# Performance work log

Hardware: AMD Instinct MI355X
Metric: run time of the kernel (lower is better)

The kernel has to match this reference:

```python
import jax, jax.numpy as jnp
import numpy as np

HEAD_DIM = 32
N_HEADS = 8
Q_DIM = 128
FF_DIM = 4 * Q_DIM
EPS = 1e-5


def layernorm(x, gamma, beta):
    mu = jnp.mean(x, axis=-1, keepdims=True)
    var = jnp.var(x, axis=-1, keepdims=True)
    return (x - mu) * jax.lax.rsqrt(var + EPS) * gamma + beta


def setup_inputs() -> dict:
    key = jax.random.key(0)
    ks = jax.random.split(key, 20)
    S, B = 1024, 16
    sc_in = 1.0 / np.sqrt(Q_DIM)
    sc_hd = 1.0 / np.sqrt(N_HEADS * HEAD_DIM)
    sc_ff = 1.0 / np.sqrt(FF_DIM)
    return {
        "sequence": jax.random.normal(ks[0], (S, B, Q_DIM), jnp.float32),
        # per-head Q/K/V projections, stacked over heads: [H, Q_dim, head_dim]
        "Wq": jax.random.uniform(ks[1], (N_HEADS, Q_DIM, HEAD_DIM), jnp.float32, -sc_in, sc_in),
        "bq": jax.random.uniform(ks[2], (N_HEADS, HEAD_DIM), jnp.float32, -sc_in, sc_in),
        "Wk": jax.random.uniform(ks[3], (N_HEADS, Q_DIM, HEAD_DIM), jnp.float32, -sc_in, sc_in),
        "bk": jax.random.uniform(ks[4], (N_HEADS, HEAD_DIM), jnp.float32, -sc_in, sc_in),
        "Wv": jax.random.uniform(ks[5], (N_HEADS, Q_DIM, HEAD_DIM), jnp.float32, -sc_in, sc_in),
        "bv": jax.random.uniform(ks[6], (N_HEADS, HEAD_DIM), jnp.float32, -sc_in, sc_in),
        # post_head_linear: [H*head_dim, Q_dim]
        "Wo": jax.random.uniform(ks[7], (N_HEADS * HEAD_DIM, Q_DIM), jnp.float32, -sc_hd, sc_hd),
        "bo": jax.random.uniform(ks[8], (Q_DIM,), jnp.float32, -sc_hd, sc_hd),
        # norm1 (note: original reuses norm1 for both layernorms)
        "gamma1": jnp.ones((Q_DIM,), jnp.float32),
        "beta1": jnp.zeros((Q_DIM,), jnp.float32),
        # FFN: Q_dim -> 4Q -> 4Q -> Q_dim
        "W1": jax.random.uniform(ks[9], (Q_DIM, FF_DIM), jnp.float32, -sc_in, sc_in),
        "b1": jax.random.uniform(ks[10], (FF_DIM,), jnp.float32, -sc_in, sc_in),
        "W2": jax.random.uniform(ks[11], (FF_DIM, FF_DIM), jnp.float32, -sc_ff, sc_ff),
        "b2": jax.random.uniform(ks[12], (FF_DIM,), jnp.float32, -sc_ff, sc_ff),
        "W3": jax.random.uniform(ks[13], (FF_DIM, Q_DIM), jnp.float32, -sc_ff, sc_ff),
        "b3": jax.random.uniform(ks[14], (Q_DIM,), jnp.float32, -sc_ff, sc_ff),
    }


def reference(sequence, Wq, bq, Wk, bk, Wv, bv, Wo, bo, gamma1, beta1, W1, b1, W2, b2, W3, b3):
    # sequence: [S, B, Q_dim] -> batch-first [B, S, Q_dim]
    x = jnp.transpose(sequence, (1, 0, 2))
    # batched per-head projections: [B, H, S, d]
    q = jnp.einsum('bsq,hqd->bhsd', x, Wq) + bq[None, :, None, :]
    k = jnp.einsum('bsq,hqd->bhsd', x, Wk) + bk[None, :, None, :]
    v = jnp.einsum('bsq,hqd->bhsd', x, Wv) + bv[None, :, None, :]
    scores = jnp.einsum('bhsd,bhtd->bhst', q, k) / np.sqrt(HEAD_DIM)
    attn = jax.nn.softmax(scores, axis=-1)
    o = jnp.einsum('bhst,bhtd->bhsd', attn, v)  # [B, H, S, d]
    B, H, S, d = o.shape
    o = jnp.transpose(o, (0, 2, 1, 3)).reshape(B, S, H * d)  # concat heads
    att_outs = o @ Wo + bo
    att_outs = layernorm(x + att_outs, gamma1, beta1)
    h = jax.nn.relu(att_outs @ W1 + b1)
    h = jax.nn.relu(h @ W2 + b2)
    h = h @ W3 + b3
    out = layernorm(att_outs + h, gamma1, beta1)  # original reuses norm1
    return jnp.transpose(out, (1, 0, 2))  # back to [S, B, Q_dim]
```

## Files before the change

kernel.cpp:

```cpp
#include <hip/hip_runtime.h>
#include <hip/hip_bf16.h>

#define S_LEN 1024
#define BATCH 16
#define QD 128
#define NH 8
#define HD 32
#define FF 512
#define NROWS (BATCH * S_LEN)
#define EPS 1e-5f

typedef __attribute__((ext_vector_type(4))) float f32x4;
typedef __attribute__((ext_vector_type(8))) short s16x8;
typedef __attribute__((ext_vector_type(4))) short s16x4;

__device__ __forceinline__ ushort f2bfu(float f) {
    union { float f; unsigned u; } v; v.f = f;
    unsigned r = (v.u + 0x7FFFu + ((v.u >> 16) & 1u)) >> 16;
    return (ushort)r;
}

__device__ __forceinline__ float exp2_fast(float x) {
#if __has_builtin(__builtin_amdgcn_exp2f)
    return __builtin_amdgcn_exp2f(x);
#else
    float r;
    asm("v_exp_f32 %0, %1" : "=v"(r) : "v"(x));
    return r;
#endif
}

__device__ __forceinline__ unsigned pk_bf16(float a, float b) {
    union { __hip_bfloat162 h; unsigned u; } c;
    c.h = __float22bfloat162_rn(make_float2(a, b));
    return c.u;
}

static __device__ __forceinline__ f32x4 mfma16(s16x4 a, s16x4 b, f32x4 c) {
#if __has_builtin(__builtin_amdgcn_mfma_f32_16x16x16bf16_1k)
    return __builtin_amdgcn_mfma_f32_16x16x16bf16_1k(a, b, c, 0, 0, 0);
#else
    asm volatile("v_mfma_f32_16x16x16_bf16 %0, %1, %2, %0" : "+v"(c) : "v"(a), "v"(b));
    return c;
#endif
}

static __device__ __forceinline__ f32x4 mfma32(s16x8 a, s16x8 b, f32x4 c) {
    return __builtin_amdgcn_mfma_f32_16x16x32_bf16(a, b, c, 0, 0, 0);
}

__device__ __forceinline__ void gl_lds16(const void* g, void* l) {
    __builtin_amdgcn_global_load_lds(
        (const __attribute__((address_space(1))) void*)g,
        (__attribute__((address_space(3))) void*)l, 16, 0, 0);
}

template <int K>
__device__ __forceinline__ void gemm_core(
    const ushort* __restrict__ act, const ushort* __restrict__ WTp,
    char* lds, int tok0, f32x4 acc[8]) {
    const int tid = threadIdx.x;
    const int w = tid >> 6, lane = tid & 63;
    const int qi = lane & 15, g = lane >> 4;
    const int r8 = tid >> 3;
    const int csw = (tid & 7) ^ (r8 & 7);
    const int wave_base = w * 1024;
    constexpr int NT = K / 64;

    auto STAGE = [&](int b, int ks) {
        char* buf = lds + b * 24576;
#pragma unroll
        for (int i = 0; i < 4; ++i)
            gl_lds16(WTp + (size_t)(i * 32 + r8) * K + ks + csw * 8,
                     buf + i * 4096 + wave_base);
#pragma unroll
        for (int j = 0; j < 2; ++j)
            gl_lds16(act + (size_t)(tok0 + j * 32 + r8) * K + ks + csw * 8,
                     buf + 16384 + j * 4096 + wave_base);
    };

    STAGE(0, 0);
    int cur = 0;
#pragma unroll 1
    for (int t = 0; t < NT; ++t) {
        if (t < NT - 1) {
            STAGE(cur ^ 1, (t + 1) * 64);
            asm volatile("s_waitcnt vmcnt(6)" ::: "memory");
        } else {
            asm volatile("s_waitcnt vmcnt(0)" ::: "memory");
        }
        __builtin_amdgcn_sched_barrier(0);
        __builtin_amdgcn_s_barrier();
        __builtin_amdgcn_sched_barrier(0);
        const char* A = lds + cur * 24576;
        const char* B = A + 16384;
        const int brow = w * 16 + qi;
        __builtin_amdgcn_s_setprio(1);
#pragma unroll
        for (int kk2 = 0; kk2 < 2; ++kk2) {
            s16x8 bfrag = *(const s16x8*)(B + brow * 128 +
                                          (((kk2 * 4 + g) ^ (brow & 7)) * 16));
#pragma unroll
            for (int f = 0; f < 8; ++f) {
                const int row = qi + 16 * f;
                s16x8 afrag = *(const s16x8*)(A + row * 128 +
                                              (((kk2 * 4 + g) ^ (row & 7)) * 16));
                acc[f] = mfma32(afrag, bfrag, acc[f]);
            }
        }
        __builtin_amdgcn_s_setprio(0);
        __builtin_amdgcn_sched_barrier(0);
        __builtin_amdgcn_s_barrier();
        __builtin_amdgcn_sched_barrier(0);
        cur ^= 1;
    }
}

__global__ __launch_bounds__(256) void prep_weights(
    const float* __restrict__ Wo, const float* __restrict__ W1,
    const float* __restrict__ W2, const float* __restrict__ W3,
    const float* __restrict__ Wq, const float* __restrict__ Wk,
    const float* __restrict__ Wv,
    ushort* __restrict__ WoT, ushort* __restrict__ W1T,
    ushort* __restrict__ W2T, ushort* __restrict__ W3T,
    ushort* __restrict__ WqkvT) {
    int idx = blockIdx.x * 256 + threadIdx.x;
    if (idx < 32768) {
        int n = idx >> 8, k = idx & 255;
        WoT[n * 256 + k] = f2bfu(Wo[k * 128 + n]);
    } else if (idx < 98304) {
        int i = idx - 32768; int n = i >> 7, k = i & 127;
        W1T[n * 128 + k] = f2bfu(W1[k * 512 + n]);
    } else if (idx < 360448) {
        int i = idx - 98304; int n = i >> 9, k = i & 511;
        W2T[n * 512 + k] = f2bfu(W2[k * 512 + n]);
    } else if (idx < 425984) {
        int i = idx - 360448; int n = i >> 9, k = i & 511;
        W3T[n * 512 + k] = f2bfu(W3[k * 128 + n]);
    } else {
        int i = idx - 425984;
        int n = i >> 7, k = i & 127;
        int p = n >> 8, h = (n >> 5) & 7, d = n & 31;
        const float* W = (p == 0) ? Wq : (p == 1) ? Wk : Wv;
        WqkvT[n * 128 + k] = f2bfu(W[(h * QD + k) * HD + d]);
    }
}

__global__ __launch_bounds__(256) void seq2bf(
    const float* __restrict__ seq, ushort* __restrict__ x_bf) {
    int t = blockIdx.x * 256 + threadIdx.x;
    int e4 = t * 4;
    int s = e4 >> 11, b = (e4 >> 7) & 15, c = e4 & 127;
    float4 v = *(const float4*)(seq + e4);
    ushort4 o = {f2bfu(v.x), f2bfu(v.y), f2bfu(v.z), f2bfu(v.w)};
    *(ushort4*)(x_bf + ((size_t)(b * 1024 + s)) * 128 + c) = o;
}

__global__ __launch_bounds__(256) void qkv_mfma(
    const ushort* __restrict__ x_bf, const ushort* __restrict__ WqkvT,
    const float* __restrict__ bq, const float* __restrict__ bk,
    const float* __restrict__ bv,
    ushort* __restrict__ q_bf, ushort* __restrict__ k_bf,
    ushort* __restrict__ vT) {
    __shared__ __align__(16) char lds[2 * 24576];
    const int lane = threadIdx.x & 63;
    const int w = threadIdx.x >> 6;
    const int qi = lane & 15, g = lane >> 4;
    const int tok0 = blockIdx.x * 64;
    const int tok = tok0 + w * 16 + qi;
    const int n0 = blockIdx.y * 128;

    f32x4 acc[8];
#pragma unroll
    for (int f = 0; f < 8; ++f) acc[f] = (f32x4){0.f, 0.f, 0.f, 0.f};
    gemm_core<128>(x_bf, WqkvT + (size_t)n0 * 128, lds, tok0, acc);

    const int b = tok >> 10, s = tok & 1023;
    const float SCALE = 0.25503491f;
    if (n0 < 256) {
#pragma unroll
        for (int f = 0; f < 8; ++f)
#pragma unroll
            for (int r = 0; r < 4; ++r) {
                int n = n0 + 16 * f + 4 * g + r;
                int h = (n >> 5) & 7, d = n & 31;
                q_bf[((size_t)(b * 8 + h) * 1024 + s) * 32 + d] =
                    f2bfu((acc[f][r] + bq[h * 32 + d]) * SCALE);
            }
    } else if (n0 < 512) {
#pragma unroll
        for (int f = 0; f < 8; ++f)
#pragma unroll
            for (int r = 0; r < 4; ++r) {
                int n = n0 + 16 * f + 4 * g + r;
                int h = (n >> 5) & 7, d = n & 31;
                k_bf[((size_t)(b * 8 + h) * 1024 + s) * 32 + d] =
                    f2bfu(acc[f][r] + bk[h * 32 + d]);
            }
    } else {
#pragma unroll
        for (int f = 0; f < 8; ++f)
#pragma unroll
            for (int r = 0; r < 4; ++r) {
                int n = n0 + 16 * f + 4 * g + r;
                int h = (n >> 5) & 7, d = n & 31;
                vT[((size_t)(b * 8 + h) * 32 + d) * 1024 + s] =
                    f2bfu(acc[f][r] + bv[h * 32 + d]);
            }
    }
}

__global__ __launch_bounds__(256) void attn_mfma(
    const ushort* __restrict__ qb, const ushort* __restrict__ kb,
    const ushort* __restrict__ vtb, ushort* __restrict__ o_bf) {
    __shared__ __align__(16) char lds[2][8192];
    const int tid = threadIdx.x;
    const int w = tid >> 6, lane = tid & 63;
    const int g = lane >> 4, qi = lane & 15;
    const int bid = blockIdx.x;
    const int swz = (bid & 7) * 256 + (bid >> 3);
    const int bh = swz >> 4;
    const int qtile = (swz & 15) * 4 + w;

    const ushort* Kb = kb + (size_t)bh * S_LEN * HD;
    const ushort* VTb = vtb + (size_t)bh * HD * S_LEN;
    const s16x8 qf = *(const s16x8*)(qb + ((size_t)bh * S_LEN + qtile * 16 + qi) * HD + g * 8);

    const int krow = tid >> 2;
    const int ksw = (tid & 3) ^ ((tid >> 3) & 3);
    const int vrow = tid >> 3;
    const int vsw = (tid & 7) ^ ((tid >> 4) & 7);
    const int wave_off = w * 1024;

#define STAGE(bufp, k0)                                                          \
    do {                                                                         \
        gl_lds16(Kb + (size_t)((k0) + krow) * HD + ksw * 8, (bufp) + wave_off);  \
        gl_lds16(VTb + (size_t)vrow * S_LEN + (k0) + vsw * 8,                    \
                 (bufp) + 4096 + wave_off);                                      \
    } while (0)

    f32x4 ot0 = {0.f, 0.f, 0.f, 0.f};
    f32x4 ot1 = {0.f, 0.f, 0.f, 0.f};
    float m_run = -1e30f, l_run = 0.f;
    const f32x4 zero = {0.f, 0.f, 0.f, 0.f};

    const int koff = (g ^ ((qi >> 1) & 3)) * 16;
    const int vs = (qi >> 1) & 7;

    STAGE(lds[0], 0);
    int cur = 0;
#pragma unroll 1
    for (int t = 0; t < 16; ++t) {
        if (t < 15) {
            STAGE(lds[cur ^ 1], (t + 1) * 64);
            asm volatile("s_waitcnt vmcnt(2)" ::: "memory");
        } else {
            asm volatile("s_waitcnt vmcnt(0)" ::: "memory");
        }
        __builtin_amdgcn_sched_barrier(0);
        __builtin_amdgcn_s_barrier();
        __builtin_amdgcn_sched_barrier(0);

        const char* kl = lds[cur];
        const char* vl = lds[cur] + 4096;
        s16x8 ka[4];
#pragma unroll
        for (int kt = 0; kt < 4; ++kt)
            ka[kt] = *(const s16x8*)(kl + (16 * kt + qi) * 64 + koff);
        s16x4 va[2][4];
#pragma unroll
        for (int h = 0; h < 2; ++h)
#pragma unroll
            for (int kt = 0; kt < 4; ++kt) {
                int c8 = 4 * kt + g;
                va[h][kt] = *(const s16x4*)(vl + (16 * h + qi) * 128 +
                                            (((c8 >> 1) ^ vs) * 16) + (c8 & 1) * 8);
            }

        f32x4 st[4];
        __builtin_amdgcn_s_setprio(1);
#pragma unroll
        for (int kt = 0; kt < 4; ++kt) st[kt] = mfma32(ka[kt], qf, zero);
        __builtin_amdgcn_s_setprio(0);

        float a0 = fmaxf(fmaxf(st[0][0], st[0][1]), fmaxf(st[0][2], st[0][3]));
        float a1 = fmaxf(fmaxf(st[1][0], st[1][1]), fmaxf(st[1][2], st[1][3]));
        float a2 = fmaxf(fmaxf(st[2][0], st[2][1]), fmaxf(st[2][2], st[2][3]));
        float a3 = fmaxf(fmaxf(st[3][0], st[3][1]), fmaxf(st[3][2], st[3][3]));
        float pmax = fmaxf(fmaxf(a0, a1), fmaxf(a2, a3));

        if (!__all(pmax <= m_run + 8.0f)) {
            float mt = pmax;
            mt = fmaxf(mt, __shfl_xor(mt, 16, 64));
            mt = fmaxf(mt, __shfl_xor(mt, 32, 64));
            float m_new = fmaxf(m_run, mt);
            float alpha = exp2_fast(m_run - m_new);
            l_run *= alpha;
#pragma unroll
            for (int r = 0; r < 4; ++r) { ot0[r] *= alpha; ot1[r] *= alpha; }
            m_run = m_new;
        }

        float p[4][4];
#pragma unroll
        for (int kt = 0; kt < 4; ++kt)
#pragma unroll
            for (int r = 0; r < 4; ++r) p[kt][r] = exp2_fast(st[kt][r] - m_run);
        float s0 = (p[0][0] + p[0][1]) + (p[0][2] + p[0][3]);
        float s1 = (p[1][0] + p[1][1]) + (p[1][2] + p[1][3]);
        float s2 = (p[2][0] + p[2][1]) + (p[2][2] + p[2][3]);
        float s3 = (p[3][0] + p[3][1]) + (p[3][2] + p[3][3]);
        l_run += (s0 + s1) + (s2 + s3);

        union { s16x4 v; uint2 u; } pb[4];
#pragma unroll
        for (int kt = 0; kt < 4; ++kt) {
            pb[kt].u.x = pk_bf16(p[kt][0], p[kt][1]);
            pb[kt].u.y = pk_bf16(p[kt][2], p[kt][3]);
        }
        __builtin_amdgcn_s_setprio(1);
#pragma unroll
        for (int kt = 0; kt < 4; ++kt) {
            ot0 = mfma16(va[0][kt], pb[kt].v, ot0);
            ot1 = mfma16(va[1][kt], pb[kt].v, ot1);
        }
        __builtin_amdgcn_s_setprio(0);

        __builtin_amdgcn_sched_barrier(0);
        __builtin_amdgcn_s_barrier();
        __builtin_amdgcn_sched_barrier(0);
        cur ^= 1;
    }
#undef STAGE

    l_run += __shfl_xor(l_run, 16, 64);
    l_run += __shfl_xor(l_run, 32, 64);
    const float inv_l = 1.0f / l_run;
    const int b = bh >> 3, head = bh & 7;
    const int qg = qtile * 16 + qi;
    ushort* orow = o_bf + ((size_t)(b * S_LEN + qg)) * (NH * HD) + head * HD;
    ushort4 ob0 = {f2bfu(ot0[0] * inv_l), f2bfu(ot0[1] * inv_l),
                   f2bfu(ot0[2] * inv_l), f2bfu(ot0[3] * inv_l)};
    ushort4 ob1 = {f2bfu(ot1[0] * inv_l), f2bfu(ot1[1] * inv_l),
                   f2bfu(ot1[2] * inv_l), f2bfu(ot1[3] * inv_l)};
    *(ushort4*)(orow + g * 4) = ob0;
    *(ushort4*)(orow + 16 + g * 4) = ob1;
}

__global__ __launch_bounds__(256) void wo_ln_mfma(
    const ushort* __restrict__ o_bf, const ushort* __restrict__ WoT,
    const float* __restrict__ bo, const float* __restrict__ seq,
    const float* __restrict__ gamma, const float* __restrict__ beta,
    float* __restrict__ att, ushort* __restrict__ att_bf) {
    __shared__ __align__(16) char lds[2 * 24576];
    const int lane = threadIdx.x & 63;
    const int w = threadIdx.x >> 6;
    const int qi = lane & 15, g = lane >> 4;
    const int tok0 = blockIdx.x * 64;
    const int tok = tok0 + w * 16 + qi;

    f32x4 acc[8];
#pragma unroll
    for (int f = 0; f < 8; ++f) acc[f] = (f32x4){0.f, 0.f, 0.f, 0.f};
    gemm_core<256>(o_bf, WoT, lds, tok0, acc);

    const int b = tok >> 10, s = tok & 1023;
    const float* xrow = seq + (size_t)(s * BATCH + b) * QD;
    float sum = 0.f, sumsq = 0.f;
#pragma unroll
    for (int f = 0; f < 8; ++f) {
        const int c = 16 * f + 4 * g;
        float4 bv = *(const float4*)(bo + c);
        float4 xv = *(const float4*)(xrow + c);
        acc[f][0] += bv.x + xv.x;
        acc[f][1] += bv.y + xv.y;
        acc[f][2] += bv.z + xv.z;
        acc[f][3] += bv.w + xv.w;
#pragma unroll
        for (int r = 0; r < 4; ++r) { sum += acc[f][r]; sumsq += acc[f][r] * acc[f][r]; }
    }
    sum += __shfl_xor(sum, 16, 64);
    sum += __shfl_xor(sum, 32, 64);
    sumsq += __shfl_xor(sumsq, 16, 64);
    sumsq += __shfl_xor(sumsq, 32, 64);
    const float mu = sum * (1.0f / QD);
    const float var = sumsq * (1.0f / QD) - mu * mu;
    const float rstd = rsqrtf(var + EPS);

#pragma unroll
    for (int f = 0; f < 8; ++f) {
        const int c = 16 * f + 4 * g;
        float4 gm = *(const float4*)(gamma + c);
        float4 bt = *(const float4*)(beta + c);
        float4 ov;
        ov.x = (acc[f][0] - mu) * rstd * gm.x + bt.x;
        ov.y = (acc[f][1] - mu) * rstd * gm.y + bt.y;
        ov.z = (acc[f][2] - mu) * rstd * gm.z + bt.z;
        ov.w = (acc[f][3] - mu) * rstd * gm.w + bt.w;
        *(float4*)(att + (size_t)tok * QD + c) = ov;
        ushort4 pv = {f2bfu(ov.x), f2bfu(ov.y), f2bfu(ov.z), f2bfu(ov.w)};
        *(ushort4*)(att_bf + (size_t)tok * QD + c) = pv;
    }
}

template <int K>
__global__ __launch_bounds__(256) void ffn_mfma(
    const ushort* __restrict__ act, const ushort* __restrict__ WT,
    const float* __restrict__ bias, ushort* __restrict__ out, int N) {
    __shared__ __align__(16) char lds[2 * 24576];
    const int lane = threadIdx.x & 63;
    const int w = threadIdx.x >> 6;
    const int qi = lane & 15, g = lane >> 4;
    const int tok0 = blockIdx.x * 64;
    const int tok = tok0 + w * 16 + qi;
    const int n0 = blockIdx.y * 128;

    f32x4 acc[8];
#pragma unroll
    for (int f = 0; f < 8; ++f) acc[f] = (f32x4){0.f, 0.f, 0.f, 0.f};
    gemm_core<K>(act, WT + (size_t)n0 * K, lds, tok0, acc);

#pragma unroll
    for (int f = 0; f < 8; ++f) {
        const int c = n0 + 16 * f + 4 * g;
        float4 bv = *(const float4*)(bias + c);
        ushort4 pv;
        pv.x = f2bfu(fmaxf(acc[f][0] + bv.x, 0.f));
        pv.y = f2bfu(fmaxf(acc[f][1] + bv.y, 0.f));
        pv.z = f2bfu(fmaxf(acc[f][2] + bv.z, 0.f));
        pv.w = f2bfu(fmaxf(acc[f][3] + bv.w, 0.f));
        *(ushort4*)(out + (size_t)tok * N + c) = pv;
    }
}

__global__ __launch_bounds__(256) void w3_ln_mfma(
    const ushort* __restrict__ h2, const ushort* __restrict__ W3T,
    const float* __restrict__ b3, const float* __restrict__ att,
    const float* __restrict__ gamma, const float* __restrict__ beta,
    float* __restrict__ out) {
    __shared__ __align__(16) char lds[2 * 24576];
    const int lane = threadIdx.x & 63;
    const int w = threadIdx.x >> 6;
    const int qi = lane & 15, g = lane >> 4;
    const int tok0 = blockIdx.x * 64;
    const int tok = tok0 + w * 16 + qi;

    f32x4 acc[8];
#pragma unroll
    for (int f = 0; f < 8; ++f) acc[f] = (f32x4){0.f, 0.f, 0.f, 0.f};
    gemm_core<512>(h2, W3T, lds, tok0, acc);

    float sum = 0.f, sumsq = 0.f;
#pragma unroll
    for (int f = 0; f < 8; ++f) {
        const int c = 16 * f + 4 * g;
        float4 bv = *(const float4*)(b3 + c);
        float4 xv = *(const float4*)(att + (size_t)tok * QD + c);
        acc[f][0] += bv.x + xv.x;
        acc[f][1] += bv.y + xv.y;
        acc[f][2] += bv.z + xv.z;
        acc[f][3] += bv.w + xv.w;
#pragma unroll
        for (int r = 0; r < 4; ++r) { sum += acc[f][r]; sumsq += acc[f][r] * acc[f][r]; }
    }
    sum += __shfl_xor(sum, 16, 64);
    sum += __shfl_xor(sum, 32, 64);
    sumsq += __shfl_xor(sumsq, 16, 64);
    sumsq += __shfl_xor(sumsq, 32, 64);
    const float mu = sum * (1.0f / QD);
    const float var = sumsq * (1.0f / QD) - mu * mu;
    const float rstd = rsqrtf(var + EPS);

    const int b = tok >> 10, s = tok & 1023;
    float* orow = out + (size_t)(s * BATCH + b) * QD;
#pragma unroll
    for (int f = 0; f < 8; ++f) {
        const int c = 16 * f + 4 * g;
        float4 gm = *(const float4*)(gamma + c);
        float4 bt = *(const float4*)(beta + c);
        float4 ov;
        ov.x = (acc[f][0] - mu) * rstd * gm.x + bt.x;
        ov.y = (acc[f][1] - mu) * rstd * gm.y + bt.y;
        ov.z = (acc[f][2] - mu) * rstd * gm.z + bt.z;
        ov.w = (acc[f][3] - mu) * rstd * gm.w + bt.w;
        *(float4*)(orow + c) = ov;
    }
}

extern "C" void kernel_launch(void* const* d_in, const int* in_sizes, int n_in,
                              void* d_out, int out_size, void* d_ws, size_t ws_size,
                              hipStream_t stream) {
    const float* seq = (const float*)d_in[0];
    const float* Wq = (const float*)d_in[1];
    const float* bq = (const float*)d_in[2];
    const float* Wk = (const float*)d_in[3];
    const float* bk = (const float*)d_in[4];
    const float* Wv = (const float*)d_in[5];
    const float* bv = (const float*)d_in[6];
    const float* Wo = (const float*)d_in[7];
    const float* bo = (const float*)d_in[8];
    const float* gamma = (const float*)d_in[9];
    const float* beta = (const float*)d_in[10];
    const float* W1 = (const float*)d_in[11];
    const float* b1 = (const float*)d_in[12];
    const float* W2 = (const float*)d_in[13];
    const float* b2 = (const float*)d_in[14];
    const float* W3 = (const float*)d_in[15];
    const float* b3 = (const float*)d_in[16];

    char* wsb = (char*)d_ws;
    ushort* q_bf  = (ushort*)(wsb);
    ushort* k_bf  = (ushort*)(wsb + (8ull << 20));
    ushort* vT    = (ushort*)(wsb + (16ull << 20));
    ushort* o_bf  = (ushort*)(wsb + (24ull << 20));
    float*  att   = (float*)(wsb + (32ull << 20));
    ushort* att_bf= (ushort*)(wsb + (40ull << 20));
    ushort* h1_bf = (ushort*)(wsb);
    ushort* h2_bf = (ushort*)(wsb + (16ull << 20));
    ushort* x_bf  = (ushort*)(wsb + (45ull << 20));
    ushort* WoT   = (ushort*)(wsb + (49ull << 20));
    ushort* W1T   = WoT + 32768;
    ushort* W2T   = W1T + 65536;
    ushort* W3T   = W2T + 262144;
    ushort* WqkvT = W3T + 65536;
    float* out = (float*)d_out;

    prep_weights<<<2048, 256, 0, stream>>>(Wo, W1, W2, W3, Wq, Wk, Wv,
                                           WoT, W1T, W2T, W3T, WqkvT);
    seq2bf<<<2048, 256, 0, stream>>>(seq, x_bf);
    qkv_mfma<<<dim3(NROWS / 64, 6), 256, 0, stream>>>(x_bf, WqkvT, bq, bk, bv,
                                                      q_bf, k_bf, vT);
    attn_mfma<<<(BATCH * NH) * 16, 256, 0, stream>>>(q_bf, k_bf, vT, o_bf);
    wo_ln_mfma<<<NROWS / 64, 256, 0, stream>>>(o_bf, WoT, bo, seq, gamma, beta, att, att_bf);
    ffn_mfma<QD><<<dim3(NROWS / 64, 4), 256, 0, stream>>>(att_bf, W1T, b1, h1_bf, FF);
    ffn_mfma<FF><<<dim3(NROWS / 64, 4), 256, 0, stream>>>(h1_bf, W2T, b2, h2_bf, FF);
    w3_ln_mfma<<<NROWS / 64, 256, 0, stream>>>(h2_bf, W3T, b3, att, gamma, beta, out);
}
```

Baseline: 116.6 us.

## Process two query tiles per wave and double KV tile size in attention

Each wave in the attention kernel now handles 32 queries (two 16-row tiles) instead of 16, so every K/V tile staged into LDS is reused across twice as many queries. The KV block per iteration grows from 64 to 128 keys, halving loop trips and barriers. The grid shrinks from 2048 to 1024 blocks. In exchange, LDS use and register pressure roughly double, which may reduce occupancy.

New measurement: 122.4 us. +4.9%, slower.

```diff
diff --git a/kernel.cpp b/kernel.cpp
--- a/kernel.cpp
+++ b/kernel.cpp
@@ -213,47 +213,56 @@
 __global__ __launch_bounds__(256) void attn_mfma(
     const ushort* __restrict__ qb, const ushort* __restrict__ kb,
     const ushort* __restrict__ vtb, ushort* __restrict__ o_bf) {
-    __shared__ __align__(16) char lds[2][8192];
+    __shared__ __align__(16) char lds[2][16384];
     const int tid = threadIdx.x;
     const int w = tid >> 6, lane = tid & 63;
     const int g = lane >> 4, qi = lane & 15;
     const int bid = blockIdx.x;
-    const int swz = (bid & 7) * 256 + (bid >> 3);
-    const int bh = swz >> 4;
-    const int qtile = (swz & 15) * 4 + w;
+    const int swz = (bid & 7) * 128 + (bid >> 3);
+    const int bh = swz >> 3;
+    const int q0 = (swz & 7) * 128 + w * 32;
 
     const ushort* Kb = kb + (size_t)bh * S_LEN * HD;
     const ushort* VTb = vtb + (size_t)bh * HD * S_LEN;
-    const s16x8 qf = *(const s16x8*)(qb + ((size_t)bh * S_LEN + qtile * 16 + qi) * HD + g * 8);
-
-    const int krow = tid >> 2;
-    const int ksw = (tid & 3) ^ ((tid >> 3) & 3);
-    const int vrow = tid >> 3;
-    const int vsw = (tid & 7) ^ ((tid >> 4) & 7);
-    const int wave_off = w * 1024;
+    const ushort* Qp = qb + ((size_t)bh * S_LEN + q0 + qi) * HD + g * 8;
+    const s16x8 qf0 = *(const s16x8*)(Qp);
+    const s16x8 qf1 = *(const s16x8*)(Qp + 16 * HD);
+
+    const int krow_l = lane >> 2;
+    const int kcsw = (lane & 3) ^ ((lane >> 3) & 3);
+    const int vrow_l = lane >> 4;
+    const int vcs = (lane & 15) ^ ((2 * w + (lane >> 5)) & 7);
 
 #define STAGE(bufp, k0)                                                          \
     do {                                                                         \
-        gl_lds16(Kb + (size_t)((k0) + krow) * HD + ksw * 8, (bufp) + wave_off);  \
-        gl_lds16(VTb + (size_t)vrow * S_LEN + (k0) + vsw * 8,                    \
-                 (bufp) + 4096 + wave_off);                                      \
+        gl_lds16(Kb + (size_t)((k0) + 16 * w + krow_l) * HD + kcsw * 8,          \
+                 (bufp) + w * 1024);                                             \
+        gl_lds16(Kb + (size_t)((k0) + 64 + 16 * w + krow_l) * HD + kcsw * 8,     \
+                 (bufp) + 4096 + w * 1024);                                      \
+        gl_lds16(VTb + (size_t)(4 * w + vrow_l) * S_LEN + (k0) + vcs * 8,        \
+                 (bufp) + 8192 + w * 1024);                                      \
+        gl_lds16(VTb + (size_t)(16 + 4 * w + vrow_l) * S_LEN + (k0) + vcs * 8,   \
+                 (bufp) + 12288 + w * 1024);                                     \
     } while (0)
 
-    f32x4 ot0 = {0.f, 0.f, 0.f, 0.f};
-    f32x4 ot1 = {0.f, 0.f, 0.f, 0.f};
-    float m_run = -1e30f, l_run = 0.f;
+    f32x4 ot[2][2];
+#pragma unroll
+    for (int qa = 0; qa < 2; ++qa)
+#pragma unroll
+        for (int h = 0; h < 2; ++h) ot[qa][h] = (f32x4){0.f, 0.f, 0.f, 0.f};
+    float m_run[2] = {-1e30f, -1e30f}, l_run[2] = {0.f, 0.f};
     const f32x4 zero = {0.f, 0.f, 0.f, 0.f};
 
     const int koff = (g ^ ((qi >> 1) & 3)) * 16;
-    const int vs = (qi >> 1) & 7;
+    const int vsw = (qi >> 1) & 7;
 
     STAGE(lds[0], 0);
     int cur = 0;
 #pragma unroll 1
-    for (int t = 0; t < 16; ++t) {
-        if (t < 15) {
-            STAGE(lds[cur ^ 1], (t + 1) * 64);
-            asm volatile("s_waitcnt vmcnt(2)" ::: "memory");
+    for (int t = 0; t < 8; ++t) {
+        if (t < 7) {
+            STAGE(lds[cur ^ 1], (t + 1) * 128);
+            asm volatile("s_waitcnt vmcnt(4)" ::: "memory");
         } else {
             asm volatile("s_waitcnt vmcnt(0)" ::: "memory");
         }
@@ -262,70 +271,78 @@
         __builtin_amdgcn_sched_barrier(0);
 
         const char* kl = lds[cur];
-        const char* vl = lds[cur] + 4096;
-        s16x8 ka[4];
-#pragma unroll
-        for (int kt = 0; kt < 4; ++kt)
+        const char* vl = lds[cur] + 8192;
+        s16x8 ka[8];
+#pragma unroll
+        for (int kt = 0; kt < 8; ++kt)
             ka[kt] = *(const s16x8*)(kl + (16 * kt + qi) * 64 + koff);
-        s16x4 va[2][4];
+        s16x4 va[2][8];
 #pragma unroll
         for (int h = 0; h < 2; ++h)
 #pragma unroll
-            for (int kt = 0; kt < 4; ++kt) {
-                int c8 = 4 * kt + g;
-                va[h][kt] = *(const s16x4*)(vl + (16 * h + qi) * 128 +
-                                            (((c8 >> 1) ^ vs) * 16) + (c8 & 1) * 8);
-            }
-
-        f32x4 st[4];
-        __builtin_amdgcn_s_setprio(1);
-#pragma unroll
-        for (int kt = 0; kt < 4; ++kt) st[kt] = mfma32(ka[kt], qf, zero);
-        __builtin_amdgcn_s_setprio(0);
-
-        float a0 = fmaxf(fmaxf(st[0][0], st[0][1]), fmaxf(st[0][2], st[0][3]));
-        float a1 = fmaxf(fmaxf(st[1][0], st[1][1]), fmaxf(st[1][2], st[1][3]));
-        float a2 = fmaxf(fmaxf(st[2][0], st[2][1]), fmaxf(st[2][2], st[2][3]));
-        float a3 = fmaxf(fmaxf(st[3][0], st[3][1]), fmaxf(st[3][2], st[3][3]));
-        float pmax = fmaxf(fmaxf(a0, a1), fmaxf(a2, a3));
-
-        if (!__all(pmax <= m_run + 8.0f)) {
-            float mt = pmax;
-            mt = fmaxf(mt, __shfl_xor(mt, 16, 64));
-            mt = fmaxf(mt, __shfl_xor(mt, 32, 64));
-            float m_new = fmaxf(m_run, mt);
-            float alpha = exp2_fast(m_run - m_new);
-            l_run *= alpha;
-#pragma unroll
-            for (int r = 0; r < 4; ++r) { ot0[r] *= alpha; ot1[r] *= alpha; }
-            m_run = m_new;
+            for (int kt = 0; kt < 8; ++kt)
+                va[h][kt] = *(const s16x4*)(vl + (16 * h + qi) * 256 +
+                                            (((2 * kt + (g >> 1)) ^ vsw) * 16) +
+                                            (g & 1) * 8);
+
+#pragma unroll
+        for (int qa = 0; qa < 2; ++qa) {
+            const s16x8 qf = qa ? qf1 : qf0;
+            f32x4 st[8];
+            __builtin_amdgcn_s_setprio(1);
+#pragma unroll
+            for (int kt = 0; kt < 8; ++kt) st[kt] = mfma32(ka[kt], qf, zero);
+            __builtin_amdgcn_s_setprio(0);
+
+            float a[8];
+#pragma unroll
+            for (int kt = 0; kt < 8; ++kt)
+                a[kt] = fmaxf(fmaxf(st[kt][0], st[kt][1]),
+                              fmaxf(st[kt][2], st[kt][3]));
+            float pmax = fmaxf(fmaxf(fmaxf(a[0], a[1]), fmaxf(a[2], a[3])),
+                               fmaxf(fmaxf(a[4], a[5]), fmaxf(a[6], a[7])));
+
+            if (!__all(pmax <= m_run[qa] + 8.0f)) {
+                float mt = pmax;
+                mt = fmaxf(mt, __shfl_xor(mt, 16, 64));
+                mt = fmaxf(mt, __shfl_xor(mt, 32, 64));
+                float m_new = fmaxf(m_run[qa], mt);
+                float alpha = exp2_fast(m_run[qa] - m_new);
+                l_run[qa] *= alpha;
+#pragma unroll
+                for (int r = 0; r < 4; ++r) {
+                    ot[qa][0][r] *= alpha;
+                    ot[qa][1][r] *= alpha;
+                }
+                m_run[qa] = m_new;
+            }
+
+#pragma unroll
+            for (int kt = 0; kt < 8; ++kt)
+#pragma unroll
+                for (int r = 0; r < 4; ++r)
+                    st[kt][r] = exp2_fast(st[kt][r] - m_run[qa]);
+            float ls = 0.f;
+#pragma unroll
+            for (int kt = 0; kt < 8; ++kt)
+                ls += (st[kt][0] + st[kt][1]) + (st[kt][2] + st[kt][3]);
+            l_run[qa] += ls;
+
+            union { s16x4 v; uint2 u; } pb[8];
+#pragma unroll
+            for (int kt = 0; kt < 8; ++kt) {
+                pb[kt].u.x = pk_bf16(st[kt][0], st[kt][1]);
+                pb[kt].u.y = pk_bf16(st[kt][2], st[kt][3]);
+            }
+            __builtin_amdgcn_s_setprio(1);
+#pragma unroll
+            for (int kt = 0; kt < 8; ++kt) {
+                ot[qa][0] = mfma16(va[0][kt], pb[kt].v, ot[qa][0]);
+                ot[qa][1] = mfma16(va[1][kt], pb[kt].v, ot[qa][1]);
+            }
+            __builtin_amdgcn_s_setprio(0);
         }
 
-        float p[4][4];
-#pragma unroll
-        for (int kt = 0; kt < 4; ++kt)
-#pragma unroll
-            for (int r = 0; r < 4; ++r) p[kt][r] = exp2_fast(st[kt][r] - m_run);
-        float s0 = (p[0][0] + p[0][1]) + (p[0][2] + p[0][3]);
-        float s1 = (p[1][0] + p[1][1]) + (p[1][2] + p[1][3]);
-        float s2 = (p[2][0] + p[2][1]) + (p[2][2] + p[2][3]);
-        float s3 = (p[3][0] + p[3][1]) + (p[3][2] + p[3][3]);
-        l_run += (s0 + s1) + (s2 + s3);
-
-        union { s16x4 v; uint2 u; } pb[4];
-#pragma unroll
-        for (int kt = 0; kt < 4; ++kt) {
-            pb[kt].u.x = pk_bf16(p[kt][0], p[kt][1]);
-            pb[kt].u.y = pk_bf16(p[kt][2], p[kt][3]);
-        }
-        __builtin_amdgcn_s_setprio(1);
-#pragma unroll
-        for (int kt = 0; kt < 4; ++kt) {
-            ot0 = mfma16(va[0][kt], pb[kt].v, ot0);
-            ot1 = mfma16(va[1][kt], pb[kt].v, ot1);
-        }
-        __builtin_amdgcn_s_setprio(0);
-
         __builtin_amdgcn_sched_barrier(0);
         __builtin_amdgcn_s_barrier();
         __builtin_amdgcn_sched_barrier(0);
@@ -333,18 +350,22 @@
     }
 #undef STAGE
 
-    l_run += __shfl_xor(l_run, 16, 64);
-    l_run += __shfl_xor(l_run, 32, 64);
-    const float inv_l = 1.0f / l_run;
     const int b = bh >> 3, head = bh & 7;
-    const int qg = qtile * 16 + qi;
-    ushort* orow = o_bf + ((size_t)(b * S_LEN + qg)) * (NH * HD) + head * HD;
-    ushort4 ob0 = {f2bfu(ot0[0] * inv_l), f2bfu(ot0[1] * inv_l),
-                   f2bfu(ot0[2] * inv_l), f2bfu(ot0[3] * inv_l)};
-    ushort4 ob1 = {f2bfu(ot1[0] * inv_l), f2bfu(ot1[1] * inv_l),
-                   f2bfu(ot1[2] * inv_l), f2bfu(ot1[3] * inv_l)};
-    *(ushort4*)(orow + g * 4) = ob0;
-    *(ushort4*)(orow + 16 + g * 4) = ob1;
+#pragma unroll
+    for (int qa = 0; qa < 2; ++qa) {
+        float l = l_run[qa];
+        l += __shfl_xor(l, 16, 64);
+        l += __shfl_xor(l, 32, 64);
+        const float inv_l = 1.0f / l;
+        const int q = q0 + qa * 16 + qi;
+        ushort* orow = o_bf + ((size_t)(b * S_LEN + q)) * (NH * HD) + head * HD;
+        ushort4 ob0 = {f2bfu(ot[qa][0][0] * inv_l), f2bfu(ot[qa][0][1] * inv_l),
+                       f2bfu(ot[qa][0][2] * inv_l), f2bfu(ot[qa][0][3] * inv_l)};
+        ushort4 ob1 = {f2bfu(ot[qa][1][0] * inv_l), f2bfu(ot[qa][1][1] * inv_l),
+                       f2bfu(ot[qa][1][2] * inv_l), f2bfu(ot[qa][1][3] * inv_l)};
+        *(ushort4*)(orow + g * 4) = ob0;
+        *(ushort4*)(orow + 16 + g * 4) = ob1;
+    }
 }
 
 __global__ __launch_bounds__(256) void wo_ln_mfma(
@@ -530,7 +551,7 @@
     seq2bf<<<2048, 256, 0, stream>>>(seq, x_bf);
     qkv_mfma<<<dim3(NROWS / 64, 6), 256, 0, stream>>>(x_bf, WqkvT, bq, bk, bv,
                                                       q_bf, k_bf, vT);
-    attn_mfma<<<(BATCH * NH) * 16, 256, 0, stream>>>(q_bf, k_bf, vT, o_bf);
+    attn_mfma<<<1024, 256, 0, stream>>>(q_bf, k_bf, vT, o_bf);
     wo_ln_mfma<<<NROWS / 64, 256, 0, stream>>>(o_bf, WoT, bo, seq, gamma, beta, att, att_bf);
     ffn_mfma<QD><<<dim3(NROWS / 64, 4), 256, 0, stream>>>(att_bf, W1T, b1, h1_bf, FF);
     ffn_mfma<FF><<<dim3(NROWS / 64, 4), 256, 0, stream>>>(h1_bf, W2T, b2, h2_bf, FF);
```
